# Kernel tuning notes

Measured on AMD Instinct MI355X. Metric: run time of the kernel, lower is better.

Reference implementation:

```python
import jax, jax.numpy as jnp
import numpy as np

B, T, F = 512, 256, 64
H = [128, 256, 128, 64]

def _glorot(key, shape):
    fan_in, fan_out = shape[0], shape[1]
    lim = np.sqrt(6.0 / (fan_in + fan_out))
    return jax.random.uniform(key, shape, jnp.float32, -lim, lim)

def setup_inputs() -> dict:
    key = jax.random.key(0)
    ks = jax.random.split(key, 16)
    inp = {"x": jax.random.normal(ks[0], (B, T, F), jnp.float32)}
    dims = [F] + H
    for i in range(4):
        inp[f"Wx{i+1}"] = _glorot(ks[1 + 3 * i], (dims[i], dims[i + 1]))
        # keras uses orthogonal recurrent init; scaled normal is an acceptable stand-in
        q, _ = jnp.linalg.qr(jax.random.normal(ks[2 + 3 * i], (dims[i + 1], dims[i + 1])))
        inp[f"Wh{i+1}"] = q.astype(jnp.float32)
        inp[f"b{i+1}"] = jnp.zeros((dims[i + 1],), jnp.float32)
    inp["Wd"] = _glorot(ks[13], (T * H[-1], 1))
    inp["bd"] = jnp.zeros((1,), jnp.float32)
    return inp

def simple_rnn(x, Wx, Wh, b):
    # x: [B, T, Fin] -> hidden sequence [B, T, H]; h_t = relu(x_t Wx + h_{t-1} Wh + b)
    xp = jnp.einsum('btf,fh->tbh', x, Wx) + b  # precompute input projection, time-major
    h0 = jnp.zeros((x.shape[0], Wh.shape[0]), x.dtype)
    def step(h, xt):
        h = jax.nn.relu(xt + h @ Wh)
        return h, h
    _, hs = jax.lax.scan(step, h0, xp)  # hs: [T, B, H]
    return jnp.transpose(hs, (1, 0, 2))

def reference(x, Wx1, Wh1, b1, Wx2, Wh2, b2, Wx3, Wh3, b3, Wx4, Wh4, b4, Wd, bd):
    h = simple_rnn(x, Wx1, Wh1, b1)   # dropout layers are identity at inference
    h = simple_rnn(h, Wx2, Wh2, b2)
    h = simple_rnn(h, Wx3, Wh3, b3)
    h = simple_rnn(h, Wx4, Wh4, b4)
    flat = h.reshape(h.shape[0], -1)  # [B, T*64]
    return flat @ Wd + bd             # [B, 1]
```

## Files before the change

kernel.cpp:

```cpp
#include <hip/hip_runtime.h>
#include <hip/hip_bf16.h>

#define BB 512
#define TT 256

typedef __attribute__((ext_vector_type(8))) short bf16x8;
typedef __attribute__((ext_vector_type(4))) float f32x4;

__device__ __forceinline__ unsigned short f2b(float f) {
    union { float f; unsigned u; } v; v.f = f;
    unsigned r = v.u + 0x7FFFu + ((v.u >> 16) & 1u);
    return (unsigned short)(r >> 16);
}
__device__ __forceinline__ float b2f(unsigned short h) {
    union { unsigned u; float f; } v; v.u = ((unsigned)h) << 16;
    return v.f;
}
__device__ __forceinline__ ushort2 pk2(float a, float b) {
    __hip_bfloat162 h = __float22bfloat162_rn(float2{a, b});
    union { __hip_bfloat162 h; ushort2 u; } v; v.h = h; return v.u;
}


__global__ __launch_bounds__(256) void cvt_tile(const float* __restrict__ x,
                                                unsigned short* __restrict__ xb) {
    const int blk = blockIdx.x;
    const int s = blk >> 8, t = blk & 255;
    const int tid = threadIdx.x;
    const int b = (tid >> 1) & 15;
    const int f0 = (tid >> 5) * 8 + (tid & 1) * 4;
    float4 v = *reinterpret_cast<const float4*>(
        &x[(((size_t)(s * 16 + b) * TT) + t) * 64 + f0]);
    ushort2 lo = pk2(v.x, v.y), hi = pk2(v.z, v.w);
    ushort4 o; o.x = lo.x; o.y = lo.y; o.z = hi.x; o.w = hi.y;
    *reinterpret_cast<ushort4*>(&xb[(size_t)blk * 1024 + tid * 4]) = o;
}

__global__ __launch_bounds__(512) __attribute__((amdgpu_waves_per_eu(2, 2))) void rnn4(
    const unsigned short* __restrict__ Xb,
    const float* __restrict__ Wx1, const float* __restrict__ Wh1, const float* __restrict__ b1,
    const float* __restrict__ Wx2, const float* __restrict__ Wh2, const float* __restrict__ b2,
    const float* __restrict__ Wx3, const float* __restrict__ Wh3, const float* __restrict__ b3,
    const float* __restrict__ Wx4, const float* __restrict__ Wh4, const float* __restrict__ b4,
    unsigned short* __restrict__ H4) {
    const int tid = threadIdx.x;
    const int s = blockIdx.x;
    const int w = tid >> 6;
    const int lane = tid & 63;
    const int l15 = lane & 15;
    const int quad = lane >> 4;
    const int rdo = quad * 128 + l15 * 8;

    __shared__ __align__(16) unsigned short hall[2][9216];

    bf16x8 wreg[48];
    f32x4 bvv[6];

#define LOADW(BASE, WP, H_, CB, KC_, MT_)                                          \
    _Pragma("unroll")                                                              \
    for (int mt = 0; mt < MT_; ++mt) {                                             \
        int m = (CB) + mt * 16 + l15;                                              \
        _Pragma("unroll")                                                          \
        for (int kc = 0; kc < KC_; ++kc)                                           \
            _Pragma("unroll")                                                      \
            for (int j = 0; j < 8; ++j)                                            \
                wreg[(BASE) + kc * MT_ + mt][j] =                                  \
                    (short)f2b(WP[(kc * 32 + quad * 8 + j) * H_ + m]);             \
    }
#define LOADBF(OFF, BP, CB, MT_)                                                   \
    _Pragma("unroll")                                                              \
    for (int mt = 0; mt < MT_; ++mt) {                                             \
        float4 t4v = *reinterpret_cast<const float4*>((BP) + (CB) + mt * 16 + quad * 4); \
        bvv[(OFF) + mt][0] = t4v.x; bvv[(OFF) + mt][1] = t4v.y;                    \
        bvv[(OFF) + mt][2] = t4v.z; bvv[(OFF) + mt][3] = t4v.w;                    \
    }

    if (w < 2) {
        LOADW(0,  Wh1, 128, w * 64, 4, 4)
        LOADW(16, Wx1, 128, w * 64, 2, 4)
        LOADW(24, Wh4, 64,  w * 32, 2, 2)
        LOADW(28, Wx4, 64,  w * 32, 4, 2)
        LOADBF(0, b1, w * 64, 4)
        LOADBF(4, b4, w * 32, 2)
    } else if (w < 6) {
        LOADW(0,  Wh2, 256, (w - 2) * 64, 8, 4)
        LOADW(32, Wx2, 256, (w - 2) * 64, 4, 4)
        LOADBF(0, b2, (w - 2) * 64, 4)
    } else {
        LOADW(0,  Wh3, 128, (w - 6) * 64, 4, 4)
        LOADW(16, Wx3, 128, (w - 6) * 64, 8, 4)
        LOADBF(0, b3, (w - 6) * 64, 4)
    }
#undef LOADW
#undef LOADBF

    for (int i = tid; i < 2 * 9216; i += 512) (&hall[0][0])[i] = 0;

    const unsigned short* Xs = Xb + (size_t)s * TT * 1024;
    unsigned short* H4s = H4 + (size_t)s * TT * 1024;

    if (w < 2) {
#pragma unroll
        for (int kx = 0; kx < 2; ++kx) {
            wreg[36 + kx] = *reinterpret_cast<const bf16x8*>(&Xs[kx * 512 + rdo]);
            wreg[38 + kx] = *reinterpret_cast<const bf16x8*>(&Xs[1024 + kx * 512 + rdo]);
        }
    }
    __syncthreads();

    const unsigned short* xp0 = Xs + 2 * 1024 + rdo;
    const unsigned short* xp1 = Xs + 3 * 1024 + rdo;

    const int wro1 = (w * 8 + (quad >> 1)) * 128 + l15 * 8 + (quad & 1) * 4;
    const int wro4 = 8192 + (w * 4 + (quad >> 1)) * 128 + l15 * 8 + (quad & 1) * 4;
    const int wro2 = 2048 + ((w - 2) * 8 + (quad >> 1)) * 128 + l15 * 8 + (quad & 1) * 4;
    const int wro3 = 6144 + ((w - 6) * 8 + (quad >> 1)) * 128 + l15 * 8 + (quad & 1) * 4;

    unsigned short* op_e = H4s + 1024 + (wro4 - 8192);
    unsigned short* op_o = H4s + (wro4 - 8192);

#define PACKMK(ACC_MT)                                                             \
    ushort2 lo = pk2(fmaxf((ACC_MT)[0], 0.f), fmaxf((ACC_MT)[1], 0.f));            \
    ushort2 hi = pk2(fmaxf((ACC_MT)[2], 0.f), fmaxf((ACC_MT)[3], 0.f));            \
    ushort4 o; o.x = lo.x; o.y = lo.y; o.z = hi.x; o.w = hi.y;

#define STEP(TAU_, RP_, WP_, XAB, XPP, OPP)                                        \
    {                                                                              \
        const int tau_ = (TAU_);                                                   \
        const unsigned short* RB = &hall[RP_][0];                                  \
        unsigned short* WB = &hall[WP_][0];                                        \
        if (w < 2) {                                                               \
            if ((unsigned)tau_ < TT) {                                     \
                f32x4 acc[4];                                                      \
                _Pragma("unroll")                                                  \
                for (int mt = 0; mt < 4; ++mt)                                     \
                    acc[mt] = __builtin_amdgcn_mfma_f32_16x16x32_bf16(             \
                        wreg[16 + mt], wreg[(XAB) + 0], bvv[mt], 0, 0, 0);         \
                _Pragma("unroll")                                                  \
                for (int mt = 0; mt < 4; ++mt)                                     \
                    acc[mt] = __builtin_amdgcn_mfma_f32_16x16x32_bf16(             \
                        wreg[20 + mt], wreg[(XAB) + 1], acc[mt], 0, 0, 0);         \
                if (tau_ + 2 < TT) {                                               \
                    wreg[(XAB) + 0] = *reinterpret_cast<const bf16x8*>(XPP);       \
                    wreg[(XAB) + 1] = *reinterpret_cast<const bf16x8*>(XPP + 512); \
                    XPP += 2048;                                                   \
                }                                                                  \
                _Pragma("unroll")                                                  \
                for (int kc = 0; kc < 4; ++kc) {                                   \
                    bf16x8 af = *reinterpret_cast<const bf16x8*>(&RB[rdo + kc * 512]); \
                    _Pragma("unroll")                                              \
                    for (int mt = 0; mt < 4; ++mt)                                 \
                        acc[mt] = __builtin_amdgcn_mfma_f32_16x16x32_bf16(         \
                            wreg[kc * 4 + mt], af, acc[mt], 0, 0, 0);              \
                }                                                                  \
                _Pragma("unroll")                                                  \
                for (int mt = 0; mt < 4; ++mt) {                                   \
                    PACKMK(acc[mt])                                                \
                    *reinterpret_cast<ushort4*>(&WB[wro1 + mt * 256]) = o;         \
                }                                                                  \
            }                                                                      \
            if ((unsigned)(tau_ - 3) < TT) {                               \
                f32x4 acc[2];                                                      \
                {                                                                  \
                    bf16x8 af0 = *reinterpret_cast<const bf16x8*>(&RB[6144 + rdo]); \
                    _Pragma("unroll")                                              \
                    for (int mt = 0; mt < 2; ++mt)                                 \
                        acc[mt] = __builtin_amdgcn_mfma_f32_16x16x32_bf16(         \
                            wreg[28 + mt], af0, bvv[4 + mt], 0, 0, 0);             \
                }                                                                  \
                _Pragma("unroll")                                                  \
                for (int kx = 1; kx < 4; ++kx) {                                   \
                    bf16x8 af = *reinterpret_cast<const bf16x8*>(&RB[6144 + rdo + kx * 512]); \
                    _Pragma("unroll")                                              \
                    for (int mt = 0; mt < 2; ++mt)                                 \
                        acc[mt] = __builtin_amdgcn_mfma_f32_16x16x32_bf16(         \
                            wreg[28 + kx * 2 + mt], af, acc[mt], 0, 0, 0);         \
                }                                                                  \
                _Pragma("unroll")                                                  \
                for (int kc = 0; kc < 2; ++kc) {                                   \
                    bf16x8 af = *reinterpret_cast<const bf16x8*>(&RB[8192 + rdo + kc * 512]); \
                    _Pragma("unroll")                                              \
                    for (int mt = 0; mt < 2; ++mt)                                 \
                        acc[mt] = __builtin_amdgcn_mfma_f32_16x16x32_bf16(         \
                            wreg[24 + kc * 2 + mt], af, acc[mt], 0, 0, 0);         \
                }                                                                  \
                _Pragma("unroll")                                                  \
                for (int mt = 0; mt < 2; ++mt) {                                   \
                    PACKMK(acc[mt])                                                \
                    *reinterpret_cast<ushort4*>(&WB[wro4 + mt * 256]) = o;         \
                    *reinterpret_cast<ushort4*>(OPP + mt * 256) = o;               \
                }                                                                  \
                OPP += 2048;                                                       \
            }                                                                      \
        } else if (w < 6) {                                                        \
            if ((unsigned)(tau_ - 1) < TT) {                               \
                f32x4 acc[4];                                                      \
                {                                                                  \
                    bf16x8 af0 = *reinterpret_cast<const bf16x8*>(&RB[rdo]);       \
                    _Pragma("unroll")                                              \
                    for (int mt = 0; mt < 4; ++mt)                                 \
                        acc[mt] = __builtin_amdgcn_mfma_f32_16x16x32_bf16(         \
                            wreg[32 + mt], af0, bvv[mt], 0, 0, 0);                 \
                }                                                                  \
                _Pragma("unroll")                                                  \
                for (int kx = 1; kx < 4; ++kx) {                                   \
                    bf16x8 af = *reinterpret_cast<const bf16x8*>(&RB[rdo + kx * 512]); \
                    _Pragma("unroll")                                              \
                    for (int mt = 0; mt < 4; ++mt)                                 \
                        acc[mt] = __builtin_amdgcn_mfma_f32_16x16x32_bf16(         \
                            wreg[32 + kx * 4 + mt], af, acc[mt], 0, 0, 0);         \
                }                                                                  \
                _Pragma("unroll")                                                  \
                for (int kc = 0; kc < 8; ++kc) {                                   \
                    bf16x8 af = *reinterpret_cast<const bf16x8*>(&RB[2048 + rdo + kc * 512]); \
                    _Pragma("unroll")                                              \
                    for (int mt = 0; mt < 4; ++mt)                                 \
                        acc[mt] = __builtin_amdgcn_mfma_f32_16x16x32_bf16(         \
                            wreg[kc * 4 + mt], af, acc[mt], 0, 0, 0);              \
                }                                                                  \
                _Pragma("unroll")                                                  \
                for (int mt = 0; mt < 4; ++mt) {                                   \
                    PACKMK(acc[mt])                                                \
                    *reinterpret_cast<ushort4*>(&WB[wro2 + mt * 256]) = o;         \
                }                                                                  \
            }                                                                      \
        } else {                                                                   \
            if ((unsigned)(tau_ - 2) < TT) {                               \
                f32x4 acc[4];                                                      \
                {                                                                  \
                    bf16x8 af0 = *reinterpret_cast<const bf16x8*>(&RB[2048 + rdo]); \
                    _Pragma("unroll")                                              \
                    for (int mt = 0; mt < 4; ++mt)                                 \
                        acc[mt] = __builtin_amdgcn_mfma_f32_16x16x32_bf16(         \
                            wreg[16 + mt], af0, bvv[mt], 0, 0, 0);                 \
                }                                                                  \
                _Pragma("unroll")                                                  \
                for (int kx = 1; kx < 8; ++kx) {                                   \
                    bf16x8 af = *reinterpret_cast<const bf16x8*>(&RB[2048 + rdo + kx * 512]); \
                    _Pragma("unroll")                                              \
                    for (int mt = 0; mt < 4; ++mt)                                 \
                        acc[mt] = __builtin_amdgcn_mfma_f32_16x16x32_bf16(         \
                            wreg[16 + kx * 4 + mt], af, acc[mt], 0, 0, 0);         \
                }                                                                  \
                _Pragma("unroll")                                                  \
                for (int kc = 0; kc < 4; ++kc) {                                   \
                    bf16x8 af = *reinterpret_cast<const bf16x8*>(&RB[6144 + rdo + kc * 512]); \
                    _Pragma("unroll")                                              \
                    for (int mt = 0; mt < 4; ++mt)                                 \
                        acc[mt] = __builtin_amdgcn_mfma_f32_16x16x32_bf16(         \
                            wreg[kc * 4 + mt], af, acc[mt], 0, 0, 0);              \
                }                                                                  \
                _Pragma("unroll")                                                  \
                for (int mt = 0; mt < 4; ++mt) {                                   \
                    PACKMK(acc[mt])                                                \
                    *reinterpret_cast<ushort4*>(&WB[wro3 + mt * 256]) = o;         \
                }                                                                  \
            }                                                                      \
        }                                                                          \
        __builtin_amdgcn_s_waitcnt(0xC07F);                                        \
        __builtin_amdgcn_s_barrier();                                              \
    }

#pragma unroll 1
    for (int tau = 0; tau < TT + 3; tau += 2) {
        STEP(tau, 0, 1, 36, xp0, op_e)
        STEP(tau + 1, 1, 0, 38, xp1, op_o)
    }
#undef STEP
#undef PACKMK
}

__global__ __launch_bounds__(256) void dense_part(const unsigned short* __restrict__ Ht,
                                                  const float* __restrict__ Wd,
                                                  const float* __restrict__ bd,
                                                  float* __restrict__ out) {
    __shared__ float red[16][17];
    const int s = blockIdx.x >> 3;
    const int tc = blockIdx.x & 7;
    const int tid = threadIdx.x;
    const int b = (tid >> 1) & 15;
    const int kbase = (tid >> 5) * 8 + (tid & 1) * 4;
    const unsigned short* base = Ht + ((size_t)s * TT + tc * 32) * 1024 + tid * 4;
    float acc = 0.f;
    for (int t = 0; t < 32; ++t) {
        ushort4 v = *reinterpret_cast<const ushort4*>(base + (size_t)t * 1024);
        const float* wd = &Wd[(tc * 32 + t) * 64 + kbase];
        acc += b2f(v.x) * wd[0] + b2f(v.y) * wd[1] + b2f(v.z) * wd[2] + b2f(v.w) * wd[3];
    }
    red[b][(tid >> 5) * 2 + (tid & 1)] = acc;
    __syncthreads();
    if (tid < 16) {
        float sum = 0.f;
#pragma unroll
        for (int j = 0; j < 16; ++j) sum += red[tid][j];
        if (tc == 0) sum += bd[0];
        atomicAdd(&out[s * 16 + tid], sum);
    }
}

extern "C" void kernel_launch(void* const* d_in, const int* in_sizes, int n_in,
                              void* d_out, int out_size, void* d_ws, size_t ws_size,
                              hipStream_t stream) {
    (void)in_sizes; (void)n_in; (void)ws_size;
    const float* x   = (const float*)d_in[0];
    const float* Wx1 = (const float*)d_in[1];
    const float* Wh1 = (const float*)d_in[2];
    const float* b1  = (const float*)d_in[3];
    const float* Wx2 = (const float*)d_in[4];
    const float* Wh2 = (const float*)d_in[5];
    const float* b2  = (const float*)d_in[6];
    const float* Wx3 = (const float*)d_in[7];
    const float* Wh3 = (const float*)d_in[8];
    const float* b3  = (const float*)d_in[9];
    const float* Wx4 = (const float*)d_in[10];
    const float* Wh4 = (const float*)d_in[11];
    const float* b4  = (const float*)d_in[12];
    const float* Wd  = (const float*)d_in[13];
    const float* bd  = (const float*)d_in[14];
    float* out = (float*)d_out;

    char* ws = (char*)d_ws;
    unsigned short* xbT = (unsigned short*)(ws);
    unsigned short* H4  = (unsigned short*)(ws + 16777216);

    hipMemsetAsync(out, 0, (size_t)out_size * sizeof(float), stream);

    cvt_tile<<<8192, 256, 0, stream>>>(x, xbT);

    rnn4<<<32, 512, 0, stream>>>(xbT, Wx1, Wh1, b1, Wx2, Wh2, b2,
                                 Wx3, Wh3, b3, Wx4, Wh4, b4, H4);

    dense_part<<<256, 256, 0, stream>>>(H4, Wd, bd, out);
}
```

Before: 422.4 us.

## Batch cvt over four timesteps, raise layer-2 wave priority, drop memset and atomics

The input conversion kernel now handles four timesteps per block, launching a quarter as many blocks. The layer-2 waves in the RNN kernel get a higher scheduling priority through s_setprio, presumably because they sit on the critical path. The output memset and the atomicAdd reduction are replaced by a partials buffer and a small final reduction kernel, trading one memset for one extra tiny launch. Most of the time is in the sequential rnn4 kernel, so these side changes can only recover a small amount.

After: 421.9 us. About the same (-0.1%).

```diff
diff --git a/kernel.cpp b/kernel.cpp
--- a/kernel.cpp
+++ b/kernel.cpp
@@ -22,18 +22,22 @@
 }
 
 
-__global__ __launch_bounds__(256) void cvt_tile(const float* __restrict__ x,
-                                                unsigned short* __restrict__ xb) {
-    const int blk = blockIdx.x;
-    const int s = blk >> 8, t = blk & 255;
+__global__ __launch_bounds__(256) void cvt_tile4(const float* __restrict__ x,
+                                                 unsigned short* __restrict__ xb) {
+    const int s = blockIdx.x >> 6;
+    const int tg = blockIdx.x & 63;
     const int tid = threadIdx.x;
     const int b = (tid >> 1) & 15;
     const int f0 = (tid >> 5) * 8 + (tid & 1) * 4;
-    float4 v = *reinterpret_cast<const float4*>(
-        &x[(((size_t)(s * 16 + b) * TT) + t) * 64 + f0]);
-    ushort2 lo = pk2(v.x, v.y), hi = pk2(v.z, v.w);
-    ushort4 o; o.x = lo.x; o.y = lo.y; o.z = hi.x; o.w = hi.y;
-    *reinterpret_cast<ushort4*>(&xb[(size_t)blk * 1024 + tid * 4]) = o;
+    const float* xrow = &x[(((size_t)(s * 16 + b) * TT) + tg * 4) * 64 + f0];
+    unsigned short* ob = &xb[((size_t)(s * TT) + tg * 4) * 1024 + tid * 4];
+#pragma unroll
+    for (int tt = 0; tt < 4; ++tt) {
+        float4 v = *reinterpret_cast<const float4*>(xrow + tt * 64);
+        ushort2 lo = pk2(v.x, v.y), hi = pk2(v.z, v.w);
+        ushort4 o; o.x = lo.x; o.y = lo.y; o.z = hi.x; o.w = hi.y;
+        *reinterpret_cast<ushort4*>(ob + tt * 1024) = o;
+    }
 }
 
 __global__ __launch_bounds__(512) __attribute__((amdgpu_waves_per_eu(2, 2))) void rnn4(
@@ -83,6 +87,7 @@
         LOADBF(0, b1, w * 64, 4)
         LOADBF(4, b4, w * 32, 2)
     } else if (w < 6) {
+        __builtin_amdgcn_s_setprio(1);
         LOADW(0,  Wh2, 256, (w - 2) * 64, 8, 4)
         LOADW(32, Wx2, 256, (w - 2) * 64, 4, 4)
         LOADBF(0, b2, (w - 2) * 64, 4)
@@ -272,8 +277,7 @@
 
 __global__ __launch_bounds__(256) void dense_part(const unsigned short* __restrict__ Ht,
                                                   const float* __restrict__ Wd,
-                                                  const float* __restrict__ bd,
-                                                  float* __restrict__ out) {
+                                                  float* __restrict__ part) {
     __shared__ float red[16][17];
     const int s = blockIdx.x >> 3;
     const int tc = blockIdx.x & 7;
@@ -293,15 +297,25 @@
         float sum = 0.f;
 #pragma unroll
         for (int j = 0; j < 16; ++j) sum += red[tid][j];
-        if (tc == 0) sum += bd[0];
-        atomicAdd(&out[s * 16 + tid], sum);
-    }
+        part[blockIdx.x * 16 + tid] = sum;
+    }
+}
+
+__global__ __launch_bounds__(512) void dense_final(const float* __restrict__ part,
+                                                   const float* __restrict__ bd,
+                                                   float* __restrict__ out) {
+    const int i = threadIdx.x;
+    const int s = i >> 4, b = i & 15;
+    float sum = bd[0];
+#pragma unroll
+    for (int tc = 0; tc < 8; ++tc) sum += part[(s * 8 + tc) * 16 + b];
+    out[i] = sum;
 }
 
 extern "C" void kernel_launch(void* const* d_in, const int* in_sizes, int n_in,
                               void* d_out, int out_size, void* d_ws, size_t ws_size,
                               hipStream_t stream) {
-    (void)in_sizes; (void)n_in; (void)ws_size;
+    (void)in_sizes; (void)n_in; (void)out_size; (void)ws_size;
     const float* x   = (const float*)d_in[0];
     const float* Wx1 = (const float*)d_in[1];
     const float* Wh1 = (const float*)d_in[2];
@@ -320,15 +334,15 @@
     float* out = (float*)d_out;
 
     char* ws = (char*)d_ws;
-    unsigned short* xbT = (unsigned short*)(ws);
-    unsigned short* H4  = (unsigned short*)(ws + 16777216);
-
-    hipMemsetAsync(out, 0, (size_t)out_size * sizeof(float), stream);
-
-    cvt_tile<<<8192, 256, 0, stream>>>(x, xbT);
+    unsigned short* xbT  = (unsigned short*)(ws);
+    unsigned short* H4   = (unsigned short*)(ws + 16777216);
+    float*          part = (float*)(ws + 2 * 16777216);
+
+    cvt_tile4<<<2048, 256, 0, stream>>>(x, xbT);
 
     rnn4<<<32, 512, 0, stream>>>(xbT, Wx1, Wh1, b1, Wx2, Wh2, b2,
                                  Wx3, Wh3, b3, Wx4, Wh4, b4, H4);
 
-    dense_part<<<256, 256, 0, stream>>>(H4, Wd, bd, out);
-}
+    dense_part<<<256, 256, 0, stream>>>(H4, Wd, part);
+    dense_final<<<1, 512, 0, stream>>>(part, bd, out);
+}
```
